# Optimization experiments

Hardware: AMD Instinct MI355X
Metric: run time of the kernel (lower is better)

## Reference

```python
import jax, jax.numpy as jnp
import numpy as np

N_SAMPLES = 2 ** 15          # 32768
STEP = 256                   # transform_step_size
WIN = 2048                   # transform/synthesis window
N_FRAMES = N_SAMPLES // STEP # 128
N_COEFFS = WIN // 2 + 1      # 1025
DILATIONS = (1, 2, 4, 8, 16, 32, 64, 1)


def hann(n):
    return 0.5 - 0.5 * jnp.cos(2.0 * jnp.pi * jnp.arange(n, dtype=jnp.float32) / n)


def transform(audio):
    # audio: (B, 1, N) -> magnitude STFT (B, 1024, 128)
    x = audio[:, 0, :]
    x = jnp.pad(x, ((0, 0), (0, WIN - STEP)))  # pad so n_frames == N_SAMPLES // STEP
    idx = np.arange(N_FRAMES)[:, None] * STEP + np.arange(WIN)[None, :]
    frames = x[:, idx] * hann(WIN)
    spec = jnp.abs(jnp.fft.rfft(frames, norm='ortho'))   # (B, F, 1025)
    return spec[..., : N_COEFFS - 1].transpose(0, 2, 1)  # (B, 1024, F)


def conv1x1(x, w, b):
    # x: (B, I, T), w: (O, I, 1), b: (O,)
    return jnp.einsum('oi,bit->bot', w[:, :, 0], x) + b[None, :, None]


def anticausal_block(x, w, b, dilation):
    # kernel_size=2 anti-causal dilated conv: looks at t and t+dilation (pad future)
    x_fut = jnp.pad(x, ((0, 0), (0, 0), (0, dilation)))[:, :, dilation:]
    y = (jnp.einsum('oi,bit->bot', w[:, :, 0], x)
         + jnp.einsum('oi,bit->bot', w[:, :, 1], x_fut)
         + b[None, :, None])
    y = jax.nn.leaky_relu(y, 0.2)
    y = y + x
    # do_norm: per-example max-norm
    y = y / (jnp.max(jnp.abs(y), axis=(1, 2), keepdims=True) + 1e-8)
    return y


def upsample_with_holes(x, desired_size):
    # zero-stuffing upsample: out[..., ::step] = x
    b, c, t = x.shape
    step = desired_size // t
    out = jnp.zeros((b, c, desired_size), x.dtype)
    return out.at[:, :, ::step].set(x)


def freq_domain_resonance(coeffs):
    # coeffs: (1, C, 1025) in [0, 1); per-frame decay = repeated spectral multiply
    c = jnp.clip(coeffs, 0.0, 0.9999)
    exps = jnp.arange(1, N_FRAMES + 1, dtype=coeffs.dtype)
    mags = c[:, :, None, :] ** exps[None, None, :, None]     # (1, C, F, 1025)
    frames = jnp.fft.irfft(mags, n=WIN) * hann(WIN)
    hop = WIN // 2
    total = hop * (N_FRAMES - 1) + WIN
    idx = np.arange(N_FRAMES)[:, None] * hop + np.arange(WIN)[None, :]
    out = jnp.zeros(frames.shape[:2] + (total,), frames.dtype)
    out = out.at[:, :, idx].add(frames)                      # overlap-add
    return out[..., :N_SAMPLES]                              # (1, C, N)


def fft_convolve(a, b):
    # circular-free conv via zero-padding to 2N, keep first N (matches repo fft_convolve)
    n = a.shape[-1]
    spec = jnp.fft.rfft(a, n=2 * n) * jnp.fft.rfft(b, n=2 * n)
    return jnp.fft.irfft(spec, n=2 * n)[..., :n]


def reference(audio, proj_in_w, proj_in_b, blocks_w, blocks_b,
              proj_sparse_w, proj_sparse_b, proj_dense_w, proj_dense_b, resonances):
    spec = transform(audio)                         # (B, 1024, 128)
    h = conv1x1(spec, proj_in_w, proj_in_b)         # (B, 32, 128)
    acc = jnp.zeros_like(h)
    for i, d in enumerate(DILATIONS):               # fixed 8-block stack
        h = anticausal_block(h, blocks_w[i], blocks_b[i], d)
        acc = acc + h
    x = conv1x1(acc, proj_sparse_w, proj_sparse_b)  # (B, 256, 128)
    sparse = jax.nn.relu(x)
    x = conv1x1(sparse, proj_dense_w, proj_dense_b) # (B, 32, 128)
    x = upsample_with_holes(x, N_SAMPLES)           # (B, 32, 32768)
    res = freq_domain_resonance(resonances)         # (1, 32, 32768), broadcast over B
    y = fft_convolve(x, res)                        # (B, 32, 32768)
    y = jnp.sum(y, axis=1, keepdims=True)           # (B, 1, 32768)
    return y, sparse


def setup_inputs() -> dict:
    key = jax.random.key(0)
    ks = jax.random.split(key, 12)
    u = lambda k, shape: jax.random.uniform(k, shape, jnp.float32, -0.05, 0.05)
    return {
        'audio': jax.random.normal(ks[0], (32, 1, N_SAMPLES), jnp.float32),
        'proj_in_w': u(ks[1], (32, 1024, 1)),
        'proj_in_b': jnp.zeros((32,), jnp.float32),
        'blocks_w': u(ks[2], (8, 32, 32, 2)),
        'blocks_b': jnp.zeros((8, 32), jnp.float32),
        'proj_sparse_w': u(ks[3], (256, 32, 1)),
        'proj_sparse_b': jnp.zeros((256,), jnp.float32),
        'proj_dense_w': u(ks[4], (32, 256, 1)),
        'proj_dense_b': jnp.zeros((32,), jnp.float32),
        'resonances': jax.random.uniform(ks[5], (1, 32, N_COEFFS), jnp.float32, 0.0, 1.0),
    }
```

## Files before the change

### kernel.cpp

```cpp
#include <hip/hip_runtime.h>

#define PI_F 3.14159265358979323846f

typedef short bf16x8 __attribute__((ext_vector_type(8)));
typedef float f32x4 __attribute__((ext_vector_type(4)));

#define MFMA16(acc, a, b) \
  acc = __builtin_amdgcn_mfma_f32_16x16x32_bf16(a, b, acc, 0, 0, 0)

#define WS_SPEC   0u
#define WS_H0     4194304u
#define WS_ACC    4325376u
#define WS_V      4456448u
#define WS_WTIN   4587520u
#define WS_WST    4620288u
#define WS_WDT    4628480u
#define WS_FRAMES 4636672u
#define WS_RES    6733824u

#define BIX(a) ((a) + ((a) >> 4))

#define BFLY(I0, I1, C, S)                                   \
  { float2 u = buf[I0]; float2 w = buf[I1];                  \
    float tr = (C) * w.x - (S) * w.y;                        \
    float ti = (C) * w.y + (S) * w.x;                        \
    buf[I0] = make_float2(u.x + tr, u.y + ti);               \
    buf[I1] = make_float2(u.x - tr, u.y - ti); }

#define CMULV(RX, RY, C, S, W) \
  { RX = (C) * (W).x - (S) * (W).y; RY = (C) * (W).y + (S) * (W).x; }

__device__ __forceinline__ void quad_bfly(float2* buf, int a, int h,
                                          float cs, float ss, float cp, float sp) {
  float2 x0 = buf[BIX(a)],         x1 = buf[BIX(a + h)];
  float2 x2 = buf[BIX(a + 2 * h)], x3 = buf[BIX(a + 3 * h)];
  float t1x = cs * x1.x - ss * x1.y, t1y = cs * x1.y + ss * x1.x;
  float t3x = cs * x3.x - ss * x3.y, t3y = cs * x3.y + ss * x3.x;
  float2 y0 = make_float2(x0.x + t1x, x0.y + t1y);
  float2 y1 = make_float2(x0.x - t1x, x0.y - t1y);
  float2 y2 = make_float2(x2.x + t3x, x2.y + t3y);
  float2 y3 = make_float2(x2.x - t3x, x2.y - t3y);
  float u2x = cp * y2.x - sp * y2.y, u2y = cp * y2.y + sp * y2.x;
  float u3x = sp * y3.x + cp * y3.y, u3y = sp * y3.y - cp * y3.x;
  buf[BIX(a)]         = make_float2(y0.x + u2x, y0.y + u2y);
  buf[BIX(a + 2 * h)] = make_float2(y0.x - u2x, y0.y - u2y);
  buf[BIX(a + h)]     = make_float2(y1.x + u3x, y1.y + u3y);
  buf[BIX(a + 3 * h)] = make_float2(y1.x - u3x, y1.y - u3y);
}

__device__ __forceinline__ void octet_bfly(float2* buf, int a, int h,
                                           float cv, float sv) {
  const float R = 0.7071067811865476f;
  float c1 = cv * cv - sv * sv, s1 = 2.f * cv * sv;
  float c2 = c1 * c1 - s1 * s1, s2 = 2.f * c1 * s1;
  float2 x0 = buf[BIX(a)],         x1 = buf[BIX(a + h)];
  float2 x2 = buf[BIX(a + 2 * h)], x3 = buf[BIX(a + 3 * h)];
  float2 x4 = buf[BIX(a + 4 * h)], x5 = buf[BIX(a + 5 * h)];
  float2 x6 = buf[BIX(a + 6 * h)], x7 = buf[BIX(a + 7 * h)];
  float tx, ty;
  CMULV(tx, ty, c2, s2, x1);
  float2 y0 = make_float2(x0.x + tx, x0.y + ty), y1 = make_float2(x0.x - tx, x0.y - ty);
  CMULV(tx, ty, c2, s2, x3);
  float2 y2 = make_float2(x2.x + tx, x2.y + ty), y3 = make_float2(x2.x - tx, x2.y - ty);
  CMULV(tx, ty, c2, s2, x5);
  float2 y4 = make_float2(x4.x + tx, x4.y + ty), y5 = make_float2(x4.x - tx, x4.y - ty);
  CMULV(tx, ty, c2, s2, x7);
  float2 y6 = make_float2(x6.x + tx, x6.y + ty), y7 = make_float2(x6.x - tx, x6.y - ty);
  CMULV(tx, ty, c1, s1, y2);
  float2 z0 = make_float2(y0.x + tx, y0.y + ty), z2 = make_float2(y0.x - tx, y0.y - ty);
  CMULV(tx, ty, c1, s1, y3);
  float2 z1 = make_float2(y1.x + ty, y1.y - tx), z3 = make_float2(y1.x - ty, y1.y + tx);
  CMULV(tx, ty, c1, s1, y6);
  float2 z4 = make_float2(y4.x + tx, y4.y + ty), z6 = make_float2(y4.x - tx, y4.y - ty);
  CMULV(tx, ty, c1, s1, y7);
  float2 z5 = make_float2(y5.x + ty, y5.y - tx), z7 = make_float2(y5.x - ty, y5.y + tx);
  float ca = R * (cv + sv), sa = R * (sv - cv);
  float cb = sv,            sb = -cv;
  float cc = R * (sv - cv), sc = -R * (cv + sv);
  CMULV(tx, ty, cv, sv, z4);
  buf[BIX(a)]         = make_float2(z0.x + tx, z0.y + ty);
  buf[BIX(a + 4 * h)] = make_float2(z0.x - tx, z0.y - ty);
  CMULV(tx, ty, ca, sa, z5);
  buf[BIX(a + h)]     = make_float2(z1.x + tx, z1.y + ty);
  buf[BIX(a + 5 * h)] = make_float2(z1.x - tx, z1.y - ty);
  CMULV(tx, ty, cb, sb, z6);
  buf[BIX(a + 2 * h)] = make_float2(z2.x + tx, z2.y + ty);
  buf[BIX(a + 6 * h)] = make_float2(z2.x - tx, z2.y - ty);
  CMULV(tx, ty, cc, sc, z7);
  buf[BIX(a + 3 * h)] = make_float2(z3.x + tx, z3.y + ty);
  buf[BIX(a + 7 * h)] = make_float2(z3.x - tx, z3.y - ty);
}

__device__ __forceinline__ void fft2048_stages(float2* buf, int tid) {
  octet_bfly(buf, tid << 3, 1, 1.f, 0.f);
  __syncthreads();
  {
    int j = tid & 7;
    int a = ((tid >> 3) << 6) + j;
    float sv, cv;
    __sincosf(-PI_F / 32.f * (float)j, &sv, &cv);
    octet_bfly(buf, a, 8, cv, sv);
  }
  __syncthreads();
  {
    int j = tid & 63;
    int a = ((tid >> 6) << 9) + j;
    float sv, cv;
    __sincosf(-PI_F / 256.f * (float)j, &sv, &cv);
    octet_bfly(buf, a, 64, cv, sv);
  }
  __syncthreads();
  for (int g = tid; g < 512; g += 256) {
    float sp, cp;
    __sincosf(-PI_F / 1024.f * (float)g, &sp, &cp);
    float c2 = cp * cp - sp * sp, s2 = 2.f * cp * sp;
    quad_bfly(buf, g, 512, c2, s2, cp, sp);
  }
  __syncthreads();
}

__global__ __launch_bounds__(256) void k_fft(const float* __restrict__ audio,
                                             const float* __restrict__ resin,
                                             const float* __restrict__ Win,
                                             const float* __restrict__ Ws,
                                             const float* __restrict__ Wd,
                                             const float* __restrict__ bwIn,
                                             float* __restrict__ spec,
                                             float* __restrict__ frames,
                                             float* __restrict__ WT,
                                             float* __restrict__ WsT,
                                             float* __restrict__ WdT,
                                             short* __restrict__ Whg,
                                             short* __restrict__ Wlg) {
  __shared__ float2 buf[2176];
  int blk = blockIdx.x;

  if (blk >= 2560) {
    int i = (blk - 2560) * 256 + threadIdx.x;
    if (i < 8192)  { int o2 = i >> 5, m = i & 31;   WsT[m * 256 + o2] = Ws[i]; }
    if (i < 8192)  { int c = i >> 8, o2 = i & 255;  WdT[o2 * 32 + c] = Wd[i]; }
    if (i < 16384) {
      int w = i & 1, m = (i >> 1) & 31, o = (i >> 6) & 31, s = i >> 11;
      float val = bwIn[i];
      unsigned bits = __float_as_uint(val);
      float rem = val - __uint_as_float(bits & 0xffff0000u);
      int row = (s * 2 + w) * 32 + o;
      Whg[row * 32 + m] = (short)(bits >> 16);
      Wlg[row * 32 + m] = (short)(__float_as_uint(rem) >> 16);
    }
    return;
  }

  if (blk < 2048) {
    int b  = blk >> 6;
    int f0 = (blk & 63) * 2;
    for (int j = threadIdx.x; j < 2048; j += 256) {
      float h = 0.5f - 0.5f * __cosf(0.0030679615757712823f * (float)j);
      int i1 = f0 * 256 + j;
      int i2 = i1 + 256;
      float a1 = (i1 < 32768) ? audio[b * 32768 + i1] : 0.f;
      float a2 = (i2 < 32768) ? audio[b * 32768 + i2] : 0.f;
      buf[BIX(__brev((unsigned)j) >> 21)] = make_float2(a1 * h, a2 * h);
    }
    __syncthreads();
    fft2048_stages(buf, threadIdx.x);
    const float scale = 0.5f * 0.022097086912079608f;
    for (int k = threadIdx.x; k < 1024; k += 256) {
      float2 zk = buf[BIX(k)];
      float2 zn = buf[BIX((2048 - k) & 2047)];
      float f1r = zk.x + zn.x, f1i = zk.y - zn.y;
      float f2r = zk.y + zn.y, f2i = zk.x - zn.x;
      spec[(b * 128 + f0) * 1024 + k]     = sqrtf(f1r * f1r + f1i * f1i) * scale;
      spec[(b * 128 + f0 + 1) * 1024 + k] = sqrtf(f2r * f2r + f2i * f2i) * scale;
    }
  } else {
    int r = blk - 2048;
    int c = r >> 4;
    int g = r & 15;
    float e1 = (float)(2 * g + 1);
    for (int k = threadIdx.x; k < 2048; k += 256) {
      int kk = (k <= 1024) ? k : 2048 - k;
      float cv = resin[c * 1025 + kk];
      cv = fminf(fmaxf(cv, 0.f), 0.9999f);
      float m1 = __powf(cv, e1);
      float m2 = m1 * cv;
      buf[BIX(__brev((unsigned)k) >> 21)] = make_float2(m1, m2);
    }
    __syncthreads();
    fft2048_stages(buf, threadIdx.x);
    for (int j = threadIdx.x; j < 2048; j += 256) {
      float h  = 0.5f - 0.5f * __cosf(0.0030679615757712823f * (float)j);
      float sc = h * (1.f / 2048.f);
      float2 z = buf[BIX(j)];
      frames[(c * 32 + 2 * g) * 2048 + j]     = z.x * sc;
      frames[(c * 32 + 2 * g + 1) * 2048 + j] = z.y * sc;
    }
  }
}

__global__ __launch_bounds__(256) void k_proj_in(const float* __restrict__ spec,
                                                 const float* __restrict__ Win,
                                                 const float* __restrict__ bias,
                                                 float* __restrict__ h0) {
  __shared__ float specL[8][1024];
  __shared__ float red[32][8][8];
  int b  = blockIdx.x >> 4;
  int t0 = (blockIdx.x & 15) * 8;
  for (int i = threadIdx.x; i < 8192; i += 256) {
    int tt = i >> 10, k = i & 1023;
    specL[tt][k] = spec[(b * 128 + t0 + tt) * 1024 + k];
  }
  __syncthreads();
  int o = threadIdx.x & 31, p = threadIdx.x >> 5;
  float part[8] = {0.f,0.f,0.f,0.f,0.f,0.f,0.f,0.f};
  const float4* Wrow = (const float4*)(Win + o * 1024);
  for (int k4 = p * 32; k4 < p * 32 + 32; ++k4) {
    float4 w4 = Wrow[k4];
    int k = k4 * 4;
#pragma unroll
    for (int tt = 0; tt < 8; ++tt) {
      float4 s4 = *(const float4*)&specL[tt][k];
      part[tt] += w4.x * s4.x + w4.y * s4.y + w4.z * s4.z + w4.w * s4.w;
    }
  }
#pragma unroll
  for (int tt = 0; tt < 8; ++tt) red[o][tt][p] = part[tt];
  __syncthreads();
  int oo = threadIdx.x >> 3, tt2 = threadIdx.x & 7;
  float s = bias[oo];
#pragma unroll
  for (int p2 = 0; p2 < 8; ++p2) s += red[oo][tt2][p2];
  h0[b * 4096 + oo * 128 + t0 + tt2] = s;
}

__global__ __launch_bounds__(1024) void k_chain(const float* __restrict__ h0,
                                                const short* __restrict__ Whg,
                                                const short* __restrict__ Wlg,
                                                const float* __restrict__ bb,
                                                float* __restrict__ accout,
                                                const float* __restrict__ frames,
                                                short* __restrict__ Bh,
                                                short* __restrict__ Bl) {
  __shared__ __align__(16) short Hh[192 * 40];
  __shared__ __align__(16) short Hl[192 * 40];
  __shared__ float Hf[128 * 33];
  __shared__ float bL[256];
  __shared__ float red[16];
  int blk = blockIdx.x, tid = threadIdx.x;

  if (blk >= 32) {
    int ubb = (blk - 32) * 4 + (tid >> 8);
    int r   = tid & 255;
    int c   = ubb >> 4, o = ubb & 15;
    bf16x8 hv, lv;
#pragma unroll
    for (int j = 0; j < 8; ++j) {
      int fo = 8 * o + j;
      int g  = fo >> 2;
      int j0 = ((fo & 3) << 8) + r;
      float val = frames[(c * 32 + g) * 2048 + j0];
      if (g > 0) val += frames[(c * 32 + g - 1) * 2048 + j0 + 1024];
      unsigned bits = __float_as_uint(val);
      float rem = val - __uint_as_float(bits & 0xffff0000u);
      hv[j] = (short)(bits >> 16);
      lv[j] = (short)(__float_as_uint(rem) >> 16);
    }
    int unit = (ubb * 16 + (r >> 4)) * 16 + (r & 15);
    ((bf16x8*)Bh)[unit] = hv;
    ((bf16x8*)Bl)[unit] = lv;
    return;
  }

  int b = blk;
  for (int i = tid; i < 4096; i += 1024) {
    int t = i & 127;
    int o = i >> 7;
    float val = h0[b * 4096 + i];
    Hf[t * 33 + o] = val;
    unsigned bits = __float_as_uint(val);
    float rem = val - __uint_as_float(bits & 0xffff0000u);
    Hh[t * 40 + o] = (short)(bits >> 16);
    Hl[t * 40 + o] = (short)(__float_as_uint(rem) >> 16);
  }
  for (int i = tid; i < 64 * 40; i += 1024) {
    Hh[128 * 40 + i] = 0;
    Hl[128 * 40 + i] = 0;
  }
  if (tid < 256) bL[tid] = bb[tid];
  __syncthreads();

  int wave = tid >> 6, lane = tid & 63;
  int quad = lane >> 4, l15 = lane & 15;
  int t0 = (wave & 7) * 16, o0 = (wave >> 3) * 16;
  int tD = t0 + quad * 4;
  int oD = o0 + l15;

  const bf16x8* Hh8 = (const bf16x8*)Hh;
  const bf16x8* Hl8 = (const bf16x8*)Hl;
  const bf16x8* Wh8 = (const bf16x8*)Whg;
  const bf16x8* Wl8 = (const bf16x8*)Wlg;

  float accsum[4] = {0.f, 0.f, 0.f, 0.f};
  const int DIL[8] = {1, 2, 4, 8, 16, 32, 64, 1};

#pragma unroll
  for (int s = 0; s < 8; ++s) {
    int arow = t0 + l15;
    int frow = arow + DIL[s];
    bf16x8 Ah = Hh8[arow * 5 + quad];
    bf16x8 Al = Hl8[arow * 5 + quad];
    bf16x8 Fh = Hh8[frow * 5 + quad];
    bf16x8 Fl = Hl8[frow * 5 + quad];
    int w0row = ((s * 2 + 0) * 32 + oD) * 4 + quad;
    int w1row = ((s * 2 + 1) * 32 + oD) * 4 + quad;
    bf16x8 B0h = Wh8[w0row], B0l = Wl8[w0row];
    bf16x8 B1h = Wh8[w1row], B1l = Wl8[w1row];
    float bias = bL[s * 32 + oD];
    f32x4 acc = {bias, bias, bias, bias};
    MFMA16(acc, Ah, B0h); MFMA16(acc, Ah, B0l); MFMA16(acc, Al, B0h);
    MFMA16(acc, Fh, B1h); MFMA16(acc, Fh, B1l); MFMA16(acc, Fl, B1h);
    float hnew[4], lmax = 0.f;
#pragma unroll
    for (int r = 0; r < 4; ++r) {
      float sv = acc[r];
      sv = (sv > 0.f) ? sv : 0.2f * sv;
      sv += Hf[(tD + r) * 33 + oD];
      hnew[r] = sv;
      lmax = fmaxf(lmax, fabsf(sv));
    }
#pragma unroll
    for (int off = 32; off > 0; off >>= 1)
      lmax = fmaxf(lmax, __shfl_down(lmax, off, 64));
    if (lane == 0) red[wave] = lmax;
    __syncthreads();
    float mx = red[0];
#pragma unroll
    for (int i = 1; i < 16; ++i) mx = fmaxf(mx, red[i]);
    float nm = 1.f / (mx + 1e-8f);
#pragma unroll
    for (int r = 0; r < 4; ++r) {
      float hv = hnew[r] * nm;
      accsum[r] += hv;
      int t = tD + r;
      Hf[t * 33 + oD] = hv;
      unsigned bits = __float_as_uint(hv);
      float rem = hv - __uint_as_float(bits & 0xffff0000u);
      Hh[t * 40 + oD] = (short)(bits >> 16);
      Hl[t * 40 + oD] = (short)(__float_as_uint(rem) >> 16);
    }
    __syncthreads();
  }
#pragma unroll
  for (int r = 0; r < 4; ++r)
    accout[b * 4096 + (tD + r) * 32 + oD] = accsum[r];
}

__global__ __launch_bounds__(256) void k_sparse_dense(const float* __restrict__ acc,
                                                      const float* __restrict__ WsT,
                                                      const float* __restrict__ bs,
                                                      const float* __restrict__ WdT,
                                                      const float* __restrict__ bd,
                                                      float* __restrict__ out_sparse,
                                                      float* __restrict__ v) {
  __shared__ float accL[8][32];
  __shared__ float sL[8][256];
  __shared__ float red[8][8][32];
  int b = blockIdx.x >> 4, tq = blockIdx.x & 15;
  int t0 = tq * 8;
  int tid = threadIdx.x;
  accL[tid >> 5][tid & 31] = acc[b * 4096 + (t0 + (tid >> 5)) * 32 + (tid & 31)];
  __syncthreads();
  float bsv = bs[tid];
  float s[8];
#pragma unroll
  for (int j = 0; j < 8; ++j) s[j] = bsv;
  for (int m = 0; m < 32; ++m) {
    float w = WsT[m * 256 + tid];
#pragma unroll
    for (int j = 0; j < 8; ++j) s[j] += w * accL[j][m];
  }
  float* os = out_sparse + b * 32768 + tid * 128 + t0;
#pragma unroll
  for (int j = 0; j < 8; ++j) {
    s[j] = fmaxf(s[j], 0.f);
    os[j] = s[j];
    sL[j][tid] = s[j];
  }
  __syncthreads();
  int c = tid & 31, p = tid >> 5;
  float pp[8] = {0.f,0.f,0.f,0.f,0.f,0.f,0.f,0.f};
  for (int jj = 0; jj < 32; ++jj) {
    int o2 = p * 32 + jj;
    float w = WdT[o2 * 32 + c];
#pragma unroll
    for (int j = 0; j < 8; ++j) pp[j] += w * sL[j][o2];
  }
#pragma unroll
  for (int j = 0; j < 8; ++j) red[p][j][c] = pp[j];
  __syncthreads();
  {
    int tt = tid >> 5, cc = tid & 31;
    float vv = bd[cc];
#pragma unroll
    for (int p2i = 0; p2i < 8; ++p2i) vv += red[p2i][tt][cc];
    v[b * 4096 + cc * 128 + t0 + tt] = vv;
  }
}

__global__ __launch_bounds__(512, 4) void k_conv(const float* __restrict__ v,
                                                 const short* __restrict__ Bh,
                                                 const short* __restrict__ Bl,
                                                 float* __restrict__ y) {
  __shared__ __align__(16) short AH[32 * 264];
  __shared__ __align__(16) short AL[32 * 264];
  __shared__ float vwin[2][16][48];

  int xcd  = blockIdx.x & 7;
  int slot = blockIdx.x >> 3;
  int e, b;
  if      (slot < 32) { e = xcd;      b = slot; }
  else if (slot < 64) { e = xcd + 8;  b = slot - 32; }
  else                { e = (xcd < 4) ? (xcd + 16) : (xcd + 12);
                        b = (xcd < 4) ? (slot - 64) : (slot - 48); }
  int j, uc;
  if      (e < 2)  { j = 0; uc = e; }
  else if (e < 6)  { j = 1; uc = e - 2; }
  else if (e < 12) { j = 2; uc = e - 6; }
  else             { j = 3; uc = e - 12; }
  int D0 = 32 * j - 16 * uc;

  for (int i = threadIdx.x; i < 1504; i += 512) {
    int ii = i % 47;
    int r  = i / 47;
    int c  = r & 15, ph = r >> 4;
    int d  = D0 - 15 + ii;
    vwin[ph][c][ii] = (d >= 0 && d < 128)
        ? v[b * 4096 + (16 * ph + c) * 128 + d] : 0.f;
  }
  __syncthreads();

  int lane = threadIdx.x & 63, wave = threadIdx.x >> 6;
  int quad = lane >> 4, l15 = lane & 15;
  int cq   = quad >> 1;
  int og   = 2 * uc + (quad & 1);
  int nt0  = wave * 2;

  f32x4 acc00 = (f32x4)0.f, acc01 = (f32x4)0.f;
  f32x4 acc10 = (f32x4)0.f, acc11 = (f32x4)0.f;

  const bf16x8* AH8 = (const bf16x8*)AH;
  const bf16x8* AL8 = (const bf16x8*)AL;
  const bf16x8* Bh8 = (const bf16x8*)Bh;
  const bf16x8* Bl8 = (const bf16x8*)Bl;
  short2* AH2 = (short2*)AH;
  short2* AL2 = (short2*)AL;

  int abase0 = (0 * 16 + l15) * 33 + quad;
  int abase1 = (1 * 16 + l15) * 33 + quad;

  bf16x8 pbh0, pbl0, pbh1, pbl1;
  {
    int bb0 = (cq * 16 + og) * 256 + l15;
    pbh0 = Bh8[bb0 + nt0 * 16];       pbl0 = Bl8[bb0 + nt0 * 16];
    pbh1 = Bh8[bb0 + (nt0 + 1) * 16]; pbl1 = Bl8[bb0 + (nt0 + 1) * 16];
  }

#pragma unroll
  for (int p = 0; p < 2; ++p) {
    for (int i = threadIdx.x; i < 4096; i += 512) {
      int kk2 = i & 127;
      int row = i >> 7;
      int cl  = kk2 >> 3;
      int uu  = (kk2 & 7) * 2;
      int ii  = row - uu + 15;
      float v0 = vwin[p][cl][ii];
      float v1 = vwin[p][cl][ii - 1];
      unsigned w0 = __float_as_uint(v0), w1 = __float_as_uint(v1);
      float r0 = v0 - __uint_as_float(w0 & 0xffff0000u);
      float r1 = v1 - __uint_as_float(w1 & 0xffff0000u);
      int u2 = row * 132 + kk2;
      AH2[u2] = make_short2((short)(w0 >> 16), (short)(w1 >> 16));
      AL2[u2] = make_short2((short)(__float_as_uint(r0) >> 16),
                            (short)(__float_as_uint(r1) >> 16));
    }
    __syncthreads();

#pragma unroll
    for (int ks = 0; ks < 8; ++ks) {
      bf16x8 bh0 = pbh0, bl0 = pbl0, bh1 = pbh1, bl1 = pbl1;
      int step = p * 8 + ks + 1;
      if (step < 16) {
        int cn  = 16 * (step >> 3) + 2 * (step & 7) + cq;
        int bbn = (cn * 16 + og) * 256 + l15;
        pbh0 = Bh8[bbn + nt0 * 16];       pbl0 = Bl8[bbn + nt0 * 16];
        pbh1 = Bh8[bbn + (nt0 + 1) * 16]; pbl1 = Bl8[bbn + (nt0 + 1) * 16];
      }
      bf16x8 ah0 = AH8[abase0 + ks * 4];
      bf16x8 al0 = AL8[abase0 + ks * 4];
      bf16x8 ah1 = AH8[abase1 + ks * 4];
      bf16x8 al1 = AL8[abase1 + ks * 4];
      MFMA16(acc00, ah0, bh0); MFMA16(acc00, ah0, bl0); MFMA16(acc00, al0, bh0);
      MFMA16(acc10, ah1, bh0); MFMA16(acc10, ah1, bl0); MFMA16(acc10, al1, bh0);
      MFMA16(acc01, ah0, bh1); MFMA16(acc01, ah0, bl1); MFMA16(acc01, al0, bh1);
      MFMA16(acc11, ah1, bh1); MFMA16(acc11, ah1, bl1); MFMA16(acc11, al1, bh1);
    }
    __syncthreads();
  }

  {
    float* yb0 = y + b * 32768 + (32 * j + 0 * 16 + quad * 4) * 256 + l15;
    float* yb1 = y + b * 32768 + (32 * j + 1 * 16 + quad * 4) * 256 + l15;
#pragma unroll
    for (int reg = 0; reg < 4; ++reg) {
      atomicAdd(yb0 + reg * 256 + (nt0 + 0) * 16, acc00[reg]);
      atomicAdd(yb0 + reg * 256 + (nt0 + 1) * 16, acc01[reg]);
      atomicAdd(yb1 + reg * 256 + (nt0 + 0) * 16, acc10[reg]);
      atomicAdd(yb1 + reg * 256 + (nt0 + 1) * 16, acc11[reg]);
    }
  }
}

extern "C" void kernel_launch(void* const* d_in, const int* in_sizes, int n_in,
                              void* d_out, int out_size, void* d_ws, size_t ws_size,
                              hipStream_t stream) {
  const float* audio = (const float*)d_in[0];
  const float* Win   = (const float*)d_in[1];
  const float* bin   = (const float*)d_in[2];
  const float* bw    = (const float*)d_in[3];
  const float* bb    = (const float*)d_in[4];
  const float* Ws    = (const float*)d_in[5];
  const float* bs    = (const float*)d_in[6];
  const float* Wd    = (const float*)d_in[7];
  const float* bd    = (const float*)d_in[8];
  const float* reson = (const float*)d_in[9];

  float* out = (float*)d_out;
  float* ws  = (float*)d_ws;

  float* spec   = ws + WS_SPEC;
  float* h0     = ws + WS_H0;
  float* accb   = ws + WS_ACC;
  float* vbuf   = ws + WS_V;
  float* WT     = ws + WS_WTIN;
  float* WsT    = ws + WS_WST;
  float* WdT    = ws + WS_WDT;
  float* frames = ws + WS_FRAMES;
  short* Bh = (short*)(ws + WS_RES);
  short* Bl = (short*)(ws + WS_RES + 524288u);
  short* Whg = (short*)(ws + WS_V);
  short* Wlg = (short*)(ws + WS_V + 8192u);

  hipMemsetAsync(d_out, 0, 1048576u * sizeof(float), stream);

  k_fft<<<2688, 256, 0, stream>>>(audio, reson, Win, Ws, Wd, bw,
                                  spec, frames, WT, WsT, WdT, Whg, Wlg);
  k_proj_in<<<512, 256, 0, stream>>>(spec, Win, bin, h0);
  k_chain<<<160, 1024, 0, stream>>>(h0, Whg, Wlg, bb, accb, frames, Bh, Bl);
  k_sparse_dense<<<512, 256, 0, stream>>>(accb, WsT, bs, WdT, bd, out + 1048576, vbuf);
  k_conv<<<640, 512, 0, stream>>>(vbuf, Bh, Bl, out);
}
```

Before: 172.4 us.

## Fuse input projection into STFT kernel, dropping spectrum round-trip and launch

The magnitude spectrum for each pair of frames stays in shared memory, and the 1024→32 input projection runs directly inside the FFT blocks, so the spectrum is never written to global memory. This removes the k_proj_in launch and the 16 MB spec write and read. In exchange, each FFT block now re-reads the full 128 KB Win matrix (through cache) for only two frames instead of eight, and adds extra barriers and shared-memory pressure to the FFT blocks.

```diff
diff --git a/kernel.cpp b/kernel.cpp
--- a/kernel.cpp
+++ b/kernel.cpp
@@ -125,14 +125,15 @@
                                              const float* __restrict__ Ws,
                                              const float* __restrict__ Wd,
                                              const float* __restrict__ bwIn,
-                                             float* __restrict__ spec,
+                                             const float* __restrict__ bin,
+                                             float* __restrict__ h0,
                                              float* __restrict__ frames,
-                                             float* __restrict__ WT,
                                              float* __restrict__ WsT,
                                              float* __restrict__ WdT,
                                              short* __restrict__ Whg,
                                              short* __restrict__ Wlg) {
   __shared__ float2 buf[2176];
+  __shared__ float red[512];
   int blk = blockIdx.x;
 
   if (blk >= 2560) {
@@ -165,13 +166,44 @@
     __syncthreads();
     fft2048_stages(buf, threadIdx.x);
     const float scale = 0.5f * 0.022097086912079608f;
-    for (int k = threadIdx.x; k < 1024; k += 256) {
+    float m1r[4], m2r[4];
+#pragma unroll
+    for (int q = 0; q < 4; ++q) {
+      int k = threadIdx.x + q * 256;
       float2 zk = buf[BIX(k)];
       float2 zn = buf[BIX((2048 - k) & 2047)];
       float f1r = zk.x + zn.x, f1i = zk.y - zn.y;
       float f2r = zk.y + zn.y, f2i = zk.x - zn.x;
-      spec[(b * 128 + f0) * 1024 + k]     = sqrtf(f1r * f1r + f1i * f1i) * scale;
-      spec[(b * 128 + f0 + 1) * 1024 + k] = sqrtf(f2r * f2r + f2i * f2i) * scale;
+      m1r[q] = sqrtf(f1r * f1r + f1i * f1i) * scale;
+      m2r[q] = sqrtf(f2r * f2r + f2i * f2i) * scale;
+    }
+    __syncthreads();
+#pragma unroll
+    for (int q = 0; q < 4; ++q) {
+      int k = threadIdx.x + q * 256;
+      buf[BIX(k)] = make_float2(m1r[q], m2r[q]);
+    }
+    __syncthreads();
+    int o = threadIdx.x & 31, p = threadIdx.x >> 5;
+    float part1 = 0.f, part2 = 0.f;
+    const float4* Wrow = (const float4*)(Win + o * 1024);
+    for (int k4 = p * 32; k4 < p * 32 + 32; ++k4) {
+      float4 w4 = Wrow[k4];
+      int k = k4 * 4;
+      float2 s0 = buf[BIX(k)],     s1 = buf[BIX(k + 1)];
+      float2 s2 = buf[BIX(k + 2)], s3 = buf[BIX(k + 3)];
+      part1 += w4.x * s0.x + w4.y * s1.x + w4.z * s2.x + w4.w * s3.x;
+      part2 += w4.x * s0.y + w4.y * s1.y + w4.z * s2.y + w4.w * s3.y;
+    }
+    red[(o * 2 + 0) * 8 + p] = part1;
+    red[(o * 2 + 1) * 8 + p] = part2;
+    __syncthreads();
+    if (threadIdx.x < 64) {
+      int oo = threadIdx.x >> 1, ff = threadIdx.x & 1;
+      float s = bin[oo];
+#pragma unroll
+      for (int p2 = 0; p2 < 8; ++p2) s += red[(oo * 2 + ff) * 8 + p2];
+      h0[b * 4096 + oo * 128 + f0 + ff] = s;
     }
   } else {
     int r = blk - 2048;
@@ -196,41 +228,6 @@
       frames[(c * 32 + 2 * g + 1) * 2048 + j] = z.y * sc;
     }
   }
-}
-
-__global__ __launch_bounds__(256) void k_proj_in(const float* __restrict__ spec,
-                                                 const float* __restrict__ Win,
-                                                 const float* __restrict__ bias,
-                                                 float* __restrict__ h0) {
-  __shared__ float specL[8][1024];
-  __shared__ float red[32][8][8];
-  int b  = blockIdx.x >> 4;
-  int t0 = (blockIdx.x & 15) * 8;
-  for (int i = threadIdx.x; i < 8192; i += 256) {
-    int tt = i >> 10, k = i & 1023;
-    specL[tt][k] = spec[(b * 128 + t0 + tt) * 1024 + k];
-  }
-  __syncthreads();
-  int o = threadIdx.x & 31, p = threadIdx.x >> 5;
-  float part[8] = {0.f,0.f,0.f,0.f,0.f,0.f,0.f,0.f};
-  const float4* Wrow = (const float4*)(Win + o * 1024);
-  for (int k4 = p * 32; k4 < p * 32 + 32; ++k4) {
-    float4 w4 = Wrow[k4];
-    int k = k4 * 4;
-#pragma unroll
-    for (int tt = 0; tt < 8; ++tt) {
-      float4 s4 = *(const float4*)&specL[tt][k];
-      part[tt] += w4.x * s4.x + w4.y * s4.y + w4.z * s4.z + w4.w * s4.w;
-    }
-  }
-#pragma unroll
-  for (int tt = 0; tt < 8; ++tt) red[o][tt][p] = part[tt];
-  __syncthreads();
-  int oo = threadIdx.x >> 3, tt2 = threadIdx.x & 7;
-  float s = bias[oo];
-#pragma unroll
-  for (int p2 = 0; p2 < 8; ++p2) s += red[oo][tt2][p2];
-  h0[b * 4096 + oo * 128 + t0 + tt2] = s;
 }
 
 __global__ __launch_bounds__(1024) void k_chain(const float* __restrict__ h0,
@@ -537,11 +534,9 @@
   float* out = (float*)d_out;
   float* ws  = (float*)d_ws;
 
-  float* spec   = ws + WS_SPEC;
   float* h0     = ws + WS_H0;
   float* accb   = ws + WS_ACC;
   float* vbuf   = ws + WS_V;
-  float* WT     = ws + WS_WTIN;
   float* WsT    = ws + WS_WST;
   float* WdT    = ws + WS_WDT;
   float* frames = ws + WS_FRAMES;
@@ -552,9 +547,8 @@
 
   hipMemsetAsync(d_out, 0, 1048576u * sizeof(float), stream);
 
-  k_fft<<<2688, 256, 0, stream>>>(audio, reson, Win, Ws, Wd, bw,
-                                  spec, frames, WT, WsT, WdT, Whg, Wlg);
-  k_proj_in<<<512, 256, 0, stream>>>(spec, Win, bin, h0);
+  k_fft<<<2688, 256, 0, stream>>>(audio, reson, Win, Ws, Wd, bw, bin,
+                                  h0, frames, WsT, WdT, Whg, Wlg);
   k_chain<<<160, 1024, 0, stream>>>(h0, Whg, Wlg, bb, accb, frames, Bh, Bl);
   k_sparse_dense<<<512, 256, 0, stream>>>(accb, WsT, bs, WdT, bd, out + 1048576, vbuf);
   k_conv<<<640, 512, 0, stream>>>(vbuf, Bh, Bl, out);
```

After: 194.3 us. 1.13x slower.
